# Kernel tuning notes

Measured on AMD Instinct MI355X. Metric: run time of the kernel, lower is better.

## Reference

```python
import jax, jax.numpy as jnp
import numpy as np

B, N = 8, 2048
D_IN, D_FEAT, H, K = 2, 30, 64, 8
D_ATT = D_IN + D_FEAT + H  # 96, per-head attention input dim
ALPHA = 0.2
NEG = -1e9


def setup_inputs() -> dict:
    key = jax.random.key(0)
    ks = jax.random.split(key, 11)
    inputs = jax.random.normal(ks[0], (B, N, D_IN), jnp.float32)
    envs_feat = jax.random.normal(ks[1], (B, N, D_FEAT), jnp.float32)
    state_t = jax.random.normal(ks[2], (B, N, H), jnp.float32)
    conn = jax.random.uniform(ks[3], (N, N)) < 0.05
    conn = conn | jnp.eye(N, dtype=bool)
    bias_mat = jnp.where(conn, 0.0, NEG).astype(jnp.float32)
    # xavier-ish init (gain 1.414)
    def xav(k, shape, fi, fo):
        lim = 1.414 * np.sqrt(6.0 / (fi + fo))
        return jax.random.uniform(k, shape, jnp.float32, -lim, lim)
    W_h = xav(ks[4], (K, D_ATT, H), D_ATT, H)      # stacked per-head W
    a1_h = xav(ks[5], (K, H), H, 1)
    a2_h = xav(ks[6], (K, H), H, 1)
    W_o = xav(ks[7], (K * H, H), K * H, H)
    a1_o = xav(ks[8], (H,), H, 1)
    a2_o = xav(ks[9], (H,), H, 1)
    return {"inputs": inputs, "envs_feat": envs_feat, "state_t": state_t,
            "bias_mat": bias_mat, "W_h": W_h, "a1_h": a1_h, "a2_h": a2_h,
            "W_o": W_o, "a1_o": a1_o, "a2_o": a2_o}


def _gat_multihead(h, bias, W, a1, a2):
    # h: [b,n,d], W: [k,d,h], a1/a2: [k,h], bias: [n,n]
    Wh = jnp.einsum('bnd,kdh->bknh', h, W)
    f1 = jnp.einsum('bknh,kh->bkn', Wh, a1)
    f2 = jnp.einsum('bknh,kh->bkn', Wh, a2)
    e = jax.nn.leaky_relu(f1[:, :, :, None] + f2[:, :, None, :], ALPHA) + bias  # [b,k,n,n]
    att = jax.nn.softmax(e, axis=-1)
    return jnp.einsum('bknm,bkmh->bknh', att, Wh)  # [b,k,n,h]


def _gat_single(h, bias, W, a1, a2):
    # h: [b,n,d], W: [d,h], a1/a2: [h]
    Wh = jnp.einsum('bnd,dh->bnh', h, W)
    f1 = Wh @ a1  # [b,n]
    f2 = Wh @ a2
    e = jax.nn.leaky_relu(f1[:, :, None] + f2[:, None, :], ALPHA) + bias  # [b,n,n]
    att = jax.nn.softmax(e, axis=-1)
    return jnp.einsum('bnm,bmh->bnh', att, Wh)


def reference(inputs, envs_feat, state_t, bias_mat, W_h, a1_h, a2_h, W_o, a1_o, a2_o):
    b, n = inputs.shape[0], inputs.shape[1]
    h = jnp.concatenate([inputs, envs_feat, state_t], axis=2)  # [b,n,D_ATT]
    hp = _gat_multihead(h, bias_mat, W_h, a1_h, a2_h)          # [b,k,n,h]
    h1 = jax.nn.elu(hp)
    h1 = jnp.transpose(h1, (0, 2, 1, 3)).reshape(b, n, -1)     # concat heads: [b,n,k*h]
    out = jax.nn.elu(_gat_single(h1, bias_mat, W_o, a1_o, a2_o))
    return out
```

## Files before the change

kernel.cpp:

```cpp
#include <hip/hip_runtime.h>
#include <hip/hip_bf16.h>
#include <math.h>

#define B   8
#define N   2048
#define DIN 2
#define DF  30
#define HH  64
#define KK  8
#define DATT 96
#define CAP 384
#define CAPL 176
#define ALPHA 0.2f

__device__ __forceinline__ float lrelu(float x) { return x > 0.f ? x : ALPHA * x; }
__device__ __forceinline__ float elu1(float x)  { return x > 0.f ? x : (__expf(x) - 1.f); }
__device__ __forceinline__ unsigned short f2bf(float x) {
    __hip_bfloat16 h = __float2bfloat16(x);
    return *reinterpret_cast<unsigned short*>(&h);
}
__device__ __forceinline__ float dot2bf(unsigned a, unsigned b, float acc) {
    asm("v_dot2_f32_bf16 %0, %1, %2, %0" : "+v"(acc) : "v"(a), "v"(b));
    return acc;
}

__global__ void k_prep(const float* __restrict__ bias, int* __restrict__ cols,
                       int* __restrict__ cnt,
                       const float* __restrict__ inp, const float* __restrict__ envs,
                       const float* __restrict__ st,  const float* __restrict__ W_h,
                       const float* __restrict__ a1,  const float* __restrict__ a2,
                       unsigned short* __restrict__ Whb,
                       float* __restrict__ f1n, float* __restrict__ f2n) {
    __shared__ float hs[32 * 100];
    int tid = threadIdx.x, lane = tid & 63, w = tid >> 6;

    if (blockIdx.x < 512) {
        int i = blockIdx.x * 4 + w;
        int c = 0;
        for (int j0 = 0; j0 < N; j0 += 64) {
            float v = bias[(size_t)i * N + j0 + lane];
            bool conn = v > -1e8f;
            unsigned long long m = __ballot(conn);
            if (conn) {
                int pos = c + __popcll(m & ((1ull << lane) - 1ull));
                if (pos < CAP) cols[i * CAP + pos] = j0 + lane;
            }
            c += __popcll(m);
        }
        if (lane == 0) cnt[i] = c < CAP ? c : CAP;
        return;
    }

    int x = blockIdx.x - 512;
    int tile = x & 63, k = (x >> 6) & 7, b = x >> 9;
    int i0 = tile * 32;

#pragma unroll
    for (int rep = 0; rep < 2; ++rep) {
        int idx = rep * 256 + tid;
        int row = idx >> 4, q = idx & 15;
        float4 v = *(const float4*)&st[(size_t)(b * N + i0 + row) * HH + q * 4];
        float* hb = &hs[row * 100 + DIN + DF + q * 4];
        hb[0] = v.x; hb[1] = v.y; hb[2] = v.z; hb[3] = v.w;
    }
#pragma unroll
    for (int rep = 0; rep < 2; ++rep) {
        int idx = rep * 256 + tid;
        if (idx < 480) {
            int row = idx / 15, q = idx % 15;
            float2 v = *(const float2*)&envs[(size_t)(b * N + i0 + row) * DF + q * 2];
            float* hb = &hs[row * 100 + DIN + q * 2];
            hb[0] = v.x; hb[1] = v.y;
        }
    }
    if (tid < 64) {
        int row = tid >> 1, q = tid & 1;
        hs[row * 100 + q] = inp[(size_t)(b * N + i0 + row) * DIN + q];
    }

    const float* Wk = W_h + (size_t)k * DATT * HH + lane;
    float Wv[DATT];
#pragma unroll
    for (int d = 0; d < DATT; ++d) Wv[d] = Wk[(size_t)d * HH];
    float a1k = a1[k * HH + lane], a2k = a2[k * HH + lane];

    __syncthreads();

    for (int rr = 0; rr < 8; ++rr) {
        int r = w * 8 + rr;
        const float* hb = &hs[r * 100];
        float acc0 = 0.f, acc1 = 0.f;
#pragma unroll
        for (int d = 0; d < DATT; d += 2) {
            float2 hv = *(const float2*)&hb[d];
            acc0 += hv.x * Wv[d];
            acc1 += hv.y * Wv[d + 1];
        }
        float acc = acc0 + acc1;
        int i = i0 + r;
        Whb[((size_t)(b * N + i)) * (KK * HH) + k * HH + lane] = f2bf(acc);
        float p1 = acc * a1k, p2 = acc * a2k;
#pragma unroll
        for (int off = 32; off; off >>= 1) {
            p1 += __shfl_xor(p1, off);
            p2 += __shfl_xor(p2, off);
        }
        if (lane == 0) {
            f1n[((size_t)(b * N + i)) * KK + k] = p1;
            f2n[((size_t)(b * N + i)) * KK + k] = p2;
        }
    }
}

__global__ void k_attn(const unsigned short* __restrict__ Whb, const float* __restrict__ f1n,
                       const float* __restrict__ f2n, const int* __restrict__ cols,
                       const int* __restrict__ cnt, unsigned short* __restrict__ h1b) {
    __shared__ unsigned short swb[4][8][200];
    __shared__ int jl[4][CAPL];
    int flat = blockIdx.y * (N / 4) + blockIdx.x;
    int b = flat & 7, tile = flat >> 3;
    int tid = threadIdx.x, lane = tid & 63, w = tid >> 6;
    int i = tile * 4 + w;
    int k = lane >> 3, q = lane & 7;

    int c = cnt[i]; if (c > CAPL) c = CAPL;
    const int* cl = cols + (size_t)i * CAP;
    for (int e = lane; e < c; e += 64) jl[w][e] = cl[e];
    if (lane == 0 && (c & 1)) jl[w][c] = 0;

    float f1k = f1n[((size_t)(b * N + i)) * KK + k];
    const float* f2b = f2n + (size_t)b * N * KK;

    float s[22];
    float mk = -1e30f;
#pragma unroll
    for (int t = 0; t < 22; ++t) {
        int e = t * 8 + q;
        int ee = e < c ? e : c - 1;
        int j = jl[w][ee];
        float sc = lrelu(f1k + f2b[j * KK + k]);
        if (e >= c) sc = -1e30f;
        s[t] = sc;
        mk = fmaxf(mk, sc);
    }
#pragma unroll
    for (int off = 4; off; off >>= 1) mk = fmaxf(mk, __shfl_xor(mk, off));

    float Zk = 0.f;
#pragma unroll
    for (int t = 0; t < 22; ++t) {
        float wt = __expf(s[t] - mk);
        Zk += wt;
        swb[w][k][t * 8 + q] = f2bf(wt);
    }
#pragma unroll
    for (int off = 4; off; off >>= 1) Zk += __shfl_xor(Zk, off);
    float invZ = 1.f / Zk;

    const char* Wp = (const char*)Whb + (size_t)b * N * 1024;
    float a0 = 0.f, a1_ = 0.f, a2_ = 0.f, a3_ = 0.f;
    float a4 = 0.f, a5 = 0.f, a6 = 0.f, a7 = 0.f;
    int lane16 = lane << 4;
    int cpad = (c + 1) & ~1;
#pragma unroll 4
    for (int e0 = 0; e0 < cpad; e0 += 2) {
        int j0 = __builtin_amdgcn_readfirstlane(jl[w][e0]);
        int j1 = __builtin_amdgcn_readfirstlane(jl[w][e0 + 1]);
        unsigned wp = *(const unsigned*)&swb[w][k][e0];
        uint4 v0 = *(const uint4*)(Wp + ((size_t)j0 << 10) + lane16);
        uint4 v1 = *(const uint4*)(Wp + ((size_t)j1 << 10) + lane16);
        a0 = dot2bf(__builtin_amdgcn_perm(v1.x, v0.x, 0x05040100u), wp, a0);
        a1_ = dot2bf(__builtin_amdgcn_perm(v1.x, v0.x, 0x07060302u), wp, a1_);
        a2_ = dot2bf(__builtin_amdgcn_perm(v1.y, v0.y, 0x05040100u), wp, a2_);
        a3_ = dot2bf(__builtin_amdgcn_perm(v1.y, v0.y, 0x07060302u), wp, a3_);
        a4 = dot2bf(__builtin_amdgcn_perm(v1.z, v0.z, 0x05040100u), wp, a4);
        a5 = dot2bf(__builtin_amdgcn_perm(v1.z, v0.z, 0x07060302u), wp, a5);
        a6 = dot2bf(__builtin_amdgcn_perm(v1.w, v0.w, 0x05040100u), wp, a6);
        a7 = dot2bf(__builtin_amdgcn_perm(v1.w, v0.w, 0x07060302u), wp, a7);
    }
    uint4 ov;
    ov.x = (unsigned)f2bf(elu1(a0 * invZ)) | ((unsigned)f2bf(elu1(a1_ * invZ)) << 16);
    ov.y = (unsigned)f2bf(elu1(a2_ * invZ)) | ((unsigned)f2bf(elu1(a3_ * invZ)) << 16);
    ov.z = (unsigned)f2bf(elu1(a4 * invZ)) | ((unsigned)f2bf(elu1(a5 * invZ)) << 16);
    ov.w = (unsigned)f2bf(elu1(a6 * invZ)) | ((unsigned)f2bf(elu1(a7 * invZ)) << 16);
    *(uint4*)&h1b[((size_t)(b * N + i)) * (KK * HH) + lane * 8] = ov;
}

__global__ void k_who(const unsigned short* __restrict__ h1b, const float* __restrict__ W_o,
                      const float* __restrict__ a1o, const float* __restrict__ a2o,
                      unsigned short* __restrict__ Whob, float* __restrict__ f1o,
                      float* __restrict__ f2o) {
    __shared__ unsigned Wsp[64][64];
    int tid = threadIdx.x, lane = tid & 63, w = tid >> 6;
    int g = lane >> 4, sub = lane & 15;
    int row = blockIdx.x * 16 + w * 4 + g;
    const unsigned short* hp = h1b + (size_t)row * (KK * HH);
    float ax = 0.f, ay = 0.f, az = 0.f, aw = 0.f;
    for (int ph = 0; ph < 4; ++ph) {
        __syncthreads();
#pragma unroll
        for (int rep = 0; rep < 16; ++rep) {
            int idx = rep * 256 + tid;
            int t = idx >> 6, h = idx & 63;
            const float* wp = W_o + (size_t)(ph * 128 + 2 * t) * HH + h;
            Wsp[t][h] = (unsigned)f2bf(wp[0]) | ((unsigned)f2bf(wp[HH]) << 16);
        }
        __syncthreads();
        uint4 hv = *(const uint4*)&hp[ph * 128 + sub * 8];
#pragma unroll
        for (int t = 0; t < 64; ++t) {
            unsigned src = (t & 3) == 0 ? hv.x : (t & 3) == 1 ? hv.y
                         : (t & 3) == 2 ? hv.z : hv.w;
            unsigned hpair = (unsigned)__shfl((int)src, t >> 2, 16);
            uint4 wv = *(const uint4*)&Wsp[t][sub * 4];
            ax = dot2bf(hpair, wv.x, ax);
            ay = dot2bf(hpair, wv.y, ay);
            az = dot2bf(hpair, wv.z, az);
            aw = dot2bf(hpair, wv.w, aw);
        }
    }
    unsigned lo = (unsigned)f2bf(ax) | ((unsigned)f2bf(ay) << 16);
    unsigned hi = (unsigned)f2bf(az) | ((unsigned)f2bf(aw) << 16);
    *(uint2*)&Whob[(size_t)row * HH + sub * 4] = make_uint2(lo, hi);
    float4 a1v = *(const float4*)&a1o[sub * 4];
    float4 a2v = *(const float4*)&a2o[sub * 4];
    float p1 = ax * a1v.x + ay * a1v.y + az * a1v.z + aw * a1v.w;
    float p2 = ax * a2v.x + ay * a2v.y + az * a2v.z + aw * a2v.w;
#pragma unroll
    for (int off = 8; off; off >>= 1) {
        p1 += __shfl_xor(p1, off);
        p2 += __shfl_xor(p2, off);
    }
    if (sub == 0) { f1o[row] = p1; f2o[row] = p2; }
}

__global__ void k_attn2(const unsigned short* __restrict__ Whob, const float* __restrict__ f1o,
                        const float* __restrict__ f2o, const int* __restrict__ cols,
                        const int* __restrict__ cnt, float* __restrict__ out) {
    __shared__ int            jo[16][184];
    __shared__ unsigned short swb2[16][184];
    int flat = blockIdx.y * 128 + blockIdx.x;
    int b = flat & 7;
    int tile = flat >> 3;
    int tid = threadIdx.x;
    int lane = tid & 63, w = tid >> 6;
    int g = lane >> 4, sub = lane & 15;
    int r = w * 4 + g;
    int i = tile * 16 + r;

    int c = cnt[i]; if (c > CAPL) c = CAPL;
    float f1i = f1o[b * N + i];
    const int* cl = cols + (size_t)i * CAP;
    const float* f2p = f2o + (size_t)b * N;

    float s2[11];
    float m = -1e30f;
#pragma unroll
    for (int t = 0; t < 11; ++t) {
        int e = t * 16 + sub;
        int ee = e < c ? e : c - 1;
        int j = cl[ee];
        if (e < c) jo[r][e] = j << 7;
        float sc = lrelu(f1i + f2p[j]);
        if (e >= c) sc = -1e30f;
        s2[t] = sc;
        m = fmaxf(m, sc);
    }
#pragma unroll
    for (int off = 8; off; off >>= 1) m = fmaxf(m, __shfl_xor(m, off));

    float Z = 0.f;
#pragma unroll
    for (int t = 0; t < 11; ++t) {
        int e = t * 16 + sub;
        float wt = __expf(s2[t] - m);
        Z += wt;
        if (e < c) swb2[r][e] = f2bf(wt);
    }
#pragma unroll
    for (int off = 8; off; off >>= 1) Z += __shfl_xor(Z, off);
    float invZ = 1.f / Z;

    if (sub == 0 && (c & 1)) { jo[r][c] = 0; swb2[r][c] = 0; }

    const char* Wp = (const char*)Whob + (size_t)b * N * 128;
    float a0 = 0.f, a1_ = 0.f, a2_ = 0.f, a3_ = 0.f;
    int lane8 = sub << 3;
    int cpad = (c + 1) & ~1;
    for (int e0 = 0; e0 < cpad; e0 += 2) {
        int2 jp = *(const int2*)&jo[r][e0];
        unsigned wp = *(const unsigned*)&swb2[r][e0];
        uint2 v0 = *(const uint2*)(Wp + jp.x + lane8);
        uint2 v1 = *(const uint2*)(Wp + jp.y + lane8);
        a0 = dot2bf(__builtin_amdgcn_perm(v1.x, v0.x, 0x05040100u), wp, a0);
        a1_ = dot2bf(__builtin_amdgcn_perm(v1.x, v0.x, 0x07060302u), wp, a1_);
        a2_ = dot2bf(__builtin_amdgcn_perm(v1.y, v0.y, 0x05040100u), wp, a2_);
        a3_ = dot2bf(__builtin_amdgcn_perm(v1.y, v0.y, 0x07060302u), wp, a3_);
    }
    float4 o;
    o.x = elu1(a0 * invZ); o.y = elu1(a1_ * invZ);
    o.z = elu1(a2_ * invZ); o.w = elu1(a3_ * invZ);
    *(float4*)&out[(size_t)(b * N + i) * HH + sub * 4] = o;
}

extern "C" void kernel_launch(void* const* d_in, const int* in_sizes, int n_in,
                              void* d_out, int out_size, void* d_ws, size_t ws_size,
                              hipStream_t stream) {
    const float* inp   = (const float*)d_in[0];
    const float* envs  = (const float*)d_in[1];
    const float* st    = (const float*)d_in[2];
    const float* bias  = (const float*)d_in[3];
    const float* W_h   = (const float*)d_in[4];
    const float* a1_h  = (const float*)d_in[5];
    const float* a2_h  = (const float*)d_in[6];
    const float* W_o   = (const float*)d_in[7];
    const float* a1_o  = (const float*)d_in[8];
    const float* a2_o  = (const float*)d_in[9];
    float* out = (float*)d_out;

    char* ws = (char*)d_ws;
    size_t off = 0;
    unsigned short* Whb  = (unsigned short*)(ws + off); off += (size_t)B * N * KK * HH * 2;
    unsigned short* h1b  = (unsigned short*)(ws + off); off += (size_t)B * N * KK * HH * 2;
    unsigned short* Whob = (unsigned short*)(ws + off); off += (size_t)B * N * HH * 2;
    float* f1n = (float*)(ws + off); off += (size_t)B * N * KK * 4;
    float* f2n = (float*)(ws + off); off += (size_t)B * N * KK * 4;
    float* f1o = (float*)(ws + off); off += (size_t)B * N * 4;
    float* f2o = (float*)(ws + off); off += (size_t)B * N * 4;
    int*   cols = (int*)(ws + off);  off += (size_t)N * CAP * 4;
    int*   cnt  = (int*)(ws + off);  off += (size_t)N * 4;

    k_prep<<<dim3(512 + 4096), dim3(256), 0, stream>>>(bias, cols, cnt,
                                                       inp, envs, st, W_h, a1_h, a2_h,
                                                       Whb, f1n, f2n);
    k_attn<<<dim3(N / 4, B), dim3(256), 0, stream>>>(Whb, f1n, f2n, cols, cnt, h1b);
    k_who<<<dim3(B * N / 16), dim3(256), 0, stream>>>(h1b, W_o, a1_o, a2_o, Whob, f1o, f2o);
    k_attn2<<<dim3(N / 16, B), dim3(256), 0, stream>>>(Whob, f1o, f2o, cols, cnt, out);
}
```

Before: 262.1 us.

## Fuse output projection into attention kernel and prepack W_o to bf16

Removes the separate k_who kernel by computing the W_o projection, f1o/f2o scores and Whob directly at the end of k_attn, using each wave's h1 row kept in shared memory. W_o is converted to bf16 pairs once in extra k_prep blocks and streamed into LDS in chunks. This drops the h1b global write and re-read and one launch. In exchange k_attn gains eight block-wide syncs, more LDS use, and every block reloads all of W_o.

```diff
diff --git a/kernel.cpp b/kernel.cpp
--- a/kernel.cpp
+++ b/kernel.cpp
@@ -29,11 +29,20 @@
                        const float* __restrict__ inp, const float* __restrict__ envs,
                        const float* __restrict__ st,  const float* __restrict__ W_h,
                        const float* __restrict__ a1,  const float* __restrict__ a2,
+                       const float* __restrict__ W_o, unsigned* __restrict__ Wop,
                        unsigned short* __restrict__ Whb,
                        float* __restrict__ f1n, float* __restrict__ f2n) {
     __shared__ float hs[32 * 100];
     int tid = threadIdx.x, lane = tid & 63, w = tid >> 6;
 
+    if (blockIdx.x >= 4608) {
+        int idx = (blockIdx.x - 4608) * 256 + tid;
+        int t = idx >> 6, h = idx & 63;
+        float w0 = W_o[(size_t)(2 * t) * HH + h];
+        float w1 = W_o[(size_t)(2 * t + 1) * HH + h];
+        Wop[idx] = (unsigned)f2bf(w0) | ((unsigned)f2bf(w1) << 16);
+        return;
+    }
     if (blockIdx.x < 512) {
         int i = blockIdx.x * 4 + w;
         int c = 0;
@@ -114,9 +123,13 @@
 
 __global__ void k_attn(const unsigned short* __restrict__ Whb, const float* __restrict__ f1n,
                        const float* __restrict__ f2n, const int* __restrict__ cols,
-                       const int* __restrict__ cnt, unsigned short* __restrict__ h1b) {
+                       const int* __restrict__ cnt, const unsigned* __restrict__ Wop,
+                       const float* __restrict__ a1o, const float* __restrict__ a2o,
+                       unsigned short* __restrict__ Whob, float* __restrict__ f1o,
+                       float* __restrict__ f2o) {
     __shared__ unsigned short swb[4][8][200];
     __shared__ int jl[4][CAPL];
+    __shared__ unsigned Wc[2048];
     int flat = blockIdx.y * (N / 4) + blockIdx.x;
     int b = flat & 7, tile = flat >> 3;
     int tid = threadIdx.x, lane = tid & 63, w = tid >> 6;
@@ -183,55 +196,31 @@
     ov.y = (unsigned)f2bf(elu1(a2_ * invZ)) | ((unsigned)f2bf(elu1(a3_ * invZ)) << 16);
     ov.z = (unsigned)f2bf(elu1(a4 * invZ)) | ((unsigned)f2bf(elu1(a5 * invZ)) << 16);
     ov.w = (unsigned)f2bf(elu1(a6 * invZ)) | ((unsigned)f2bf(elu1(a7 * invZ)) << 16);
-    *(uint4*)&h1b[((size_t)(b * N + i)) * (KK * HH) + lane * 8] = ov;
-}
-
-__global__ void k_who(const unsigned short* __restrict__ h1b, const float* __restrict__ W_o,
-                      const float* __restrict__ a1o, const float* __restrict__ a2o,
-                      unsigned short* __restrict__ Whob, float* __restrict__ f1o,
-                      float* __restrict__ f2o) {
-    __shared__ unsigned Wsp[64][64];
-    int tid = threadIdx.x, lane = tid & 63, w = tid >> 6;
-    int g = lane >> 4, sub = lane & 15;
-    int row = blockIdx.x * 16 + w * 4 + g;
-    const unsigned short* hp = h1b + (size_t)row * (KK * HH);
-    float ax = 0.f, ay = 0.f, az = 0.f, aw = 0.f;
-    for (int ph = 0; ph < 4; ++ph) {
+    unsigned* h1p = (unsigned*)&swb[w][0][0];
+    *(uint4*)&h1p[lane * 4] = ov;
+
+    float ao = 0.f;
+#pragma unroll 1
+    for (int chk = 0; chk < 8; ++chk) {
         __syncthreads();
 #pragma unroll
-        for (int rep = 0; rep < 16; ++rep) {
-            int idx = rep * 256 + tid;
-            int t = idx >> 6, h = idx & 63;
-            const float* wp = W_o + (size_t)(ph * 128 + 2 * t) * HH + h;
-            Wsp[t][h] = (unsigned)f2bf(wp[0]) | ((unsigned)f2bf(wp[HH]) << 16);
-        }
+        for (int rep = 0; rep < 8; ++rep)
+            Wc[rep * 256 + tid] = Wop[chk * 2048 + rep * 256 + tid];
         __syncthreads();
-        uint4 hv = *(const uint4*)&hp[ph * 128 + sub * 8];
-#pragma unroll
-        for (int t = 0; t < 64; ++t) {
-            unsigned src = (t & 3) == 0 ? hv.x : (t & 3) == 1 ? hv.y
-                         : (t & 3) == 2 ? hv.z : hv.w;
-            unsigned hpair = (unsigned)__shfl((int)src, t >> 2, 16);
-            uint4 wv = *(const uint4*)&Wsp[t][sub * 4];
-            ax = dot2bf(hpair, wv.x, ax);
-            ay = dot2bf(hpair, wv.y, ay);
-            az = dot2bf(hpair, wv.z, az);
-            aw = dot2bf(hpair, wv.w, aw);
-        }
-    }
-    unsigned lo = (unsigned)f2bf(ax) | ((unsigned)f2bf(ay) << 16);
-    unsigned hi = (unsigned)f2bf(az) | ((unsigned)f2bf(aw) << 16);
-    *(uint2*)&Whob[(size_t)row * HH + sub * 4] = make_uint2(lo, hi);
-    float4 a1v = *(const float4*)&a1o[sub * 4];
-    float4 a2v = *(const float4*)&a2o[sub * 4];
-    float p1 = ax * a1v.x + ay * a1v.y + az * a1v.z + aw * a1v.w;
-    float p2 = ax * a2v.x + ay * a2v.y + az * a2v.z + aw * a2v.w;
-#pragma unroll
-    for (int off = 8; off; off >>= 1) {
+#pragma unroll
+        for (int t = 0; t < 32; ++t) {
+            unsigned hpair = h1p[chk * 32 + t];
+            ao = dot2bf(hpair, Wc[t * 64 + lane], ao);
+        }
+    }
+    Whob[((size_t)(b * N + i)) * HH + lane] = f2bf(ao);
+    float p1 = ao * a1o[lane], p2 = ao * a2o[lane];
+#pragma unroll
+    for (int off = 32; off; off >>= 1) {
         p1 += __shfl_xor(p1, off);
         p2 += __shfl_xor(p2, off);
     }
-    if (sub == 0) { f1o[row] = p1; f2o[row] = p2; }
+    if (lane == 0) { f1o[b * N + i] = p1; f2o[b * N + i] = p2; }
 }
 
 __global__ void k_attn2(const unsigned short* __restrict__ Whob, const float* __restrict__ f1o,
@@ -321,8 +310,8 @@
     char* ws = (char*)d_ws;
     size_t off = 0;
     unsigned short* Whb  = (unsigned short*)(ws + off); off += (size_t)B * N * KK * HH * 2;
-    unsigned short* h1b  = (unsigned short*)(ws + off); off += (size_t)B * N * KK * HH * 2;
     unsigned short* Whob = (unsigned short*)(ws + off); off += (size_t)B * N * HH * 2;
+    unsigned* Wop = (unsigned*)(ws + off); off += (size_t)256 * HH * 4;
     float* f1n = (float*)(ws + off); off += (size_t)B * N * KK * 4;
     float* f2n = (float*)(ws + off); off += (size_t)B * N * KK * 4;
     float* f1o = (float*)(ws + off); off += (size_t)B * N * 4;
@@ -330,10 +319,10 @@
     int*   cols = (int*)(ws + off);  off += (size_t)N * CAP * 4;
     int*   cnt  = (int*)(ws + off);  off += (size_t)N * 4;
 
-    k_prep<<<dim3(512 + 4096), dim3(256), 0, stream>>>(bias, cols, cnt,
-                                                       inp, envs, st, W_h, a1_h, a2_h,
-                                                       Whb, f1n, f2n);
-    k_attn<<<dim3(N / 4, B), dim3(256), 0, stream>>>(Whb, f1n, f2n, cols, cnt, h1b);
-    k_who<<<dim3(B * N / 16), dim3(256), 0, stream>>>(h1b, W_o, a1_o, a2_o, Whob, f1o, f2o);
+    k_prep<<<dim3(4672), dim3(256), 0, stream>>>(bias, cols, cnt,
+                                                 inp, envs, st, W_h, a1_h, a2_h,
+                                                 W_o, Wop, Whb, f1n, f2n);
+    k_attn<<<dim3(N / 4, B), dim3(256), 0, stream>>>(Whb, f1n, f2n, cols, cnt,
+                                                     Wop, a1_o, a2_o, Whob, f1o, f2o);
     k_attn2<<<dim3(N / 16, B), dim3(256), 0, stream>>>(Whob, f1o, f2o, cols, cnt, out);
 }
```

Result: no change. 257.3 us (-1.8%).
